# Performance work log

Measured on AMD Instinct MI355X. Metric: run time of the kernel, lower is better.

Reference implementation:

```python
import jax, jax.numpy as jnp
import numpy as np

EMBED_DIM = 1024
NUM_HEADS = 16
HEAD_DIM = EMBED_DIM // NUM_HEADS


def setup_inputs() -> dict:
    key = jax.random.key(0)
    ks = jax.random.split(key, 5)
    T, B, E = 2048, 2, EMBED_DIM
    s = 1.0 / np.sqrt(E)
    return {
        "x": jax.random.normal(ks[0], (T, B, E), jnp.float32),
        "wq": jax.random.normal(ks[1], (E, E), jnp.float32) * s,
        "bq": jnp.zeros((E,), jnp.float32),
        "wk": jax.random.normal(ks[2], (E, E), jnp.float32) * s,
        "bk": jnp.zeros((E,), jnp.float32),
        "wv": jax.random.normal(ks[3], (E, E), jnp.float32) * s,
        "bv": jnp.zeros((E,), jnp.float32),
        "wo": jax.random.normal(ks[4], (E, E), jnp.float32) * s,
        "bo": jnp.zeros((E,), jnp.float32),
    }


def reference(x, wq, bq, wk, bk, wv, bv, wo, bo):
    # x: [T, B, E] (Time x Batch x Channel), self-attention: query = key = value = x
    T, B, E = x.shape
    H, D = NUM_HEADS, HEAD_DIM
    scaling = D ** -0.5
    # Linear projections (torch Linear: y = x @ W.T + b)
    q = (jnp.einsum('tbe,fe->tbf', x, wq) + bq) * scaling
    k = jnp.einsum('tbe,fe->tbf', x, wk) + bk
    v = jnp.einsum('tbe,fe->tbf', x, wv) + bv
    # reshape to [B*H, T, D] equivalent -> use [B, H, T, D]
    q = q.reshape(T, B, H, D).transpose(1, 2, 0, 3)  # [B,H,T,D]
    k = k.reshape(T, B, H, D).transpose(1, 2, 0, 3)
    v = v.reshape(T, B, H, D).transpose(1, 2, 0, 3)
    # scores: [B,H,T,S], fp32 softmax
    scores = jnp.einsum('bhtd,bhsd->bhts', q, k)
    probs = jax.nn.softmax(scores.astype(jnp.float32), axis=-1).astype(x.dtype)
    attn = jnp.einsum('bhts,bhsd->bhtd', probs, v)  # [B,H,T,D]
    attn = attn.transpose(2, 0, 1, 3).reshape(T, B, E)
    out = jnp.einsum('tbe,fe->tbf', attn, wo) + bo
    return out
```

## Files before the change

### kernel.cpp

```cpp
#include <hip/hip_runtime.h>
#include <cstddef>
#include <cstdint>

#define T_DIM 2048
#define E_DIM 1024
#define M_DIM 4096

typedef __attribute__((ext_vector_type(8))) short short8;
typedef __attribute__((ext_vector_type(8))) _Float16 half8;
typedef __attribute__((ext_vector_type(4))) float f32x4;

__device__ __forceinline__ short f16_bits(float v) {
  return __builtin_bit_cast(short, (_Float16)v);
}
__device__ __forceinline__ unsigned int pk2(float a, float b) {
  return __builtin_bit_cast(unsigned int, __builtin_amdgcn_cvt_pkrtz(a, b));
}
__device__ __forceinline__ half8 h8(short8 s) { return __builtin_bit_cast(half8, s); }

__device__ __forceinline__ void gl_lds16(const short* g, const short* l) {
  __builtin_amdgcn_global_load_lds(
      (const __attribute__((address_space(1))) unsigned int*)g,
      (__attribute__((address_space(3))) unsigned int*)l, 16, 0, 0);
}

__global__ __launch_bounds__(256) void convert_all(
    const float* __restrict__ x, const float* __restrict__ wq,
    const float* __restrict__ wk, const float* __restrict__ wv,
    const float* __restrict__ wo,
    short* __restrict__ xh, short* __restrict__ wqh, short* __restrict__ wkh,
    short* __restrict__ wvh, short* __restrict__ woh)
{
  const int bid = blockIdx.x;
  const float* in; short* hi; int base;
  if (bid < 4096)      { in = x;  hi = xh;  base = 0;    }
  else if (bid < 5120) { in = wq; hi = wqh; base = 4096; }
  else if (bid < 6144) { in = wk; hi = wkh; base = 5120; }
  else if (bid < 7168) { in = wv; hi = wvh; base = 6144; }
  else                 { in = wo; hi = woh; base = 7168; }
  const int i = (bid - base) * 256 + threadIdx.x;
  float4 v = ((const float4*)in)[i];
  uint2 p;
  p.x = (unsigned short)f16_bits(v.x) | ((unsigned int)(unsigned short)f16_bits(v.y) << 16);
  p.y = (unsigned short)f16_bits(v.z) | ((unsigned int)(unsigned short)f16_bits(v.w) << 16);
  ((uint2*)hi)[i] = p;
}

__global__ __launch_bounds__(256) void gemm_qkv(
    const short* __restrict__ xh,
    const short* __restrict__ wqh, const short* __restrict__ wkh,
    const short* __restrict__ wvh,
    const float* __restrict__ bq, const float* __restrict__ bk,
    const float* __restrict__ bv,
    short* __restrict__ qo, short* __restrict__ ko, short* __restrict__ vto)
{
  __shared__ __align__(16) short smem[128 * 32 * 2];
  short* Ah = smem;
  short* Wh = smem + 128 * 32;
  const int tid = threadIdx.x;
  const int lane = tid & 63;
  const int w = tid >> 6;
  const int quad = lane >> 4;
  const int l15 = lane & 15;
  const int sel = blockIdx.x >> 3;
  const int n0 = (blockIdx.x & 7) * 128;
  const int m0 = blockIdx.y * 128;

  const short* wsel = sel == 0 ? wqh : sel == 1 ? wkh : wvh;
  const float* bias = sel == 0 ? bq : sel == 1 ? bk : bv;
  const float scale = sel == 0 ? 0.125f * 1.44269504088896f : 1.0f;

  const short* gsrc = (w < 2) ? xh : wsel;
  short* lbuf = (w < 2) ? Ah : Wh;
  const int rbase = (w < 2) ? m0 : n0;
  const int jb = (w & 1) * 4;
  const int lrow = lane >> 2;
  const int gphys = lane & 3;

  f32x4 zero = {0.f, 0.f, 0.f, 0.f};
  f32x4 acc[4][4];
#pragma unroll
  for (int i = 0; i < 4; ++i)
#pragma unroll
    for (int j = 0; j < 4; ++j) acc[i][j] = zero;

  const int wm = w & 1, wn = w >> 1;

  for (int k0 = 0; k0 < E_DIM; k0 += 32) {
    __syncthreads();
#pragma unroll
    for (int jj = 0; jj < 4; ++jj) {
      int j = jb + jj;
      int r = j * 16 + lrow;
      int gl = (gphys - (r >> 1)) & 3;
      gl_lds16(gsrc + (size_t)(rbase + r) * E_DIM + k0 + gl * 8, lbuf + j * 512);
    }
    __syncthreads();
    short8 ahf[4];
#pragma unroll
    for (int i = 0; i < 4; ++i) {
      int r = wm * 64 + i * 16 + l15;
      int idx = r * 32 + ((quad + (r >> 1)) & 3) * 8;
      ahf[i] = *(const short8*)&Ah[idx];
    }
#pragma unroll
    for (int j = 0; j < 4; ++j) {
      int r = wn * 64 + j * 16 + l15;
      int idx = r * 32 + ((quad + (r >> 1)) & 3) * 8;
      short8 bhf = *(const short8*)&Wh[idx];
#pragma unroll
      for (int i = 0; i < 4; ++i)
        acc[i][j] = __builtin_amdgcn_mfma_f32_16x16x32_f16(h8(ahf[i]), h8(bhf), acc[i][j], 0, 0, 0);
    }
  }

  if (sel < 2) {
#pragma unroll
    for (int j = 0; j < 4; ++j) {
      const int gc = n0 + wn * 64 + j * 16 + l15;
      const float bb = bias[gc];
      const int h = gc >> 6, d = gc & 63;
      short* dst = sel == 0 ? qo : ko;
#pragma unroll
      for (int i = 0; i < 4; ++i)
#pragma unroll
        for (int reg = 0; reg < 4; ++reg) {
          const int gm = m0 + wm * 64 + i * 16 + quad * 4 + reg;
          const float val = (acc[i][j][reg] + bb) * scale;
          const int t = gm >> 1, b = gm & 1;
          dst[((size_t)(b * 16 + h) * T_DIM + t) * 64 + d] = f16_bits(val);
        }
    }
  } else {
    short* Tb = smem;
    const int by = blockIdx.y;
#pragma unroll
    for (int R = 0; R < 2; ++R) {
      __syncthreads();
      if (wn == R) {
#pragma unroll
        for (int j = 0; j < 4; ++j) {
          const int nl = j * 16 + l15;
          const int gc = n0 + R * 64 + nl;
          const float bb = bias[gc];
#pragma unroll
          for (int i = 0; i < 4; ++i) {
            const int tp = wm * 32 + i * 8 + quad * 2;
            unsigned int lo = pk2(acc[i][j][0] + bb, acc[i][j][2] + bb);
            unsigned int hi = pk2(acc[i][j][1] + bb, acc[i][j][3] + bb);
            const int g0 = tp >> 3;
            const int sub = tp & 7;
            *(unsigned int*)&Tb[nl * 128 + ((g0 + nl) & 15) * 8 + sub] = lo;
            *(unsigned int*)&Tb[nl * 128 + ((g0 + 8 + nl) & 15) * 8 + sub] = hi;
          }
        }
      }
      __syncthreads();
#pragma unroll
      for (int ii = 0; ii < 4; ++ii) {
        const int n = w * 16 + ii * 4 + quad;
        const int g = (l15 - n) & 15;
        short8 vvec = *(const short8*)&Tb[n * 128 + l15 * 8];
        const int gc = n0 + R * 64 + n;
        const int h = gc >> 6, d = gc & 63;
        const int b = g >> 3;
        const int t = by * 64 + (g & 7) * 8;
        *(short8*)&vto[((size_t)(b * 16 + h) * 64 + d) * T_DIM + t] = vvec;
      }
    }
  }
}

__global__ __launch_bounds__(256) void gemm_out(
    const short* __restrict__ attn, const short* __restrict__ woh,
    const float* __restrict__ bo, float* __restrict__ out)
{
  __shared__ __align__(16) short Ah[128 * 32], Wh[128 * 32];
  const int tid = threadIdx.x;
  const int lane = tid & 63;
  const int w = tid >> 6;
  const int quad = lane >> 4;
  const int l15 = lane & 15;
  const int n0 = blockIdx.x * 128;
  const int m0 = blockIdx.y * 128;

  const short* gsrc = (w < 2) ? attn : woh;
  short* lbuf = (w < 2) ? Ah : Wh;
  const int rbase = (w < 2) ? m0 : n0;
  const int jb = (w & 1) * 4;
  const int lrow = lane >> 2;
  const int gphys = lane & 3;

  f32x4 zero = {0.f, 0.f, 0.f, 0.f};
  f32x4 acc[4][4];
#pragma unroll
  for (int i = 0; i < 4; ++i)
#pragma unroll
    for (int j = 0; j < 4; ++j) acc[i][j] = zero;

  const int wm = w & 1, wn = w >> 1;

  for (int k0 = 0; k0 < E_DIM; k0 += 32) {
    __syncthreads();
#pragma unroll
    for (int jj = 0; jj < 4; ++jj) {
      int j = jb + jj;
      int r = j * 16 + lrow;
      int gl = (gphys - (r >> 1)) & 3;
      gl_lds16(gsrc + (size_t)(rbase + r) * E_DIM + k0 + gl * 8, lbuf + j * 512);
    }
    __syncthreads();
    short8 ahf[4];
#pragma unroll
    for (int i = 0; i < 4; ++i) {
      int r = wm * 64 + i * 16 + l15;
      int idx = r * 32 + ((quad + (r >> 1)) & 3) * 8;
      ahf[i] = *(const short8*)&Ah[idx];
    }
#pragma unroll
    for (int j = 0; j < 4; ++j) {
      int r = wn * 64 + j * 16 + l15;
      int idx = r * 32 + ((quad + (r >> 1)) & 3) * 8;
      short8 bhf = *(const short8*)&Wh[idx];
#pragma unroll
      for (int i = 0; i < 4; ++i)
        acc[i][j] = __builtin_amdgcn_mfma_f32_16x16x32_f16(h8(ahf[i]), h8(bhf), acc[i][j], 0, 0, 0);
    }
  }

#pragma unroll
  for (int j = 0; j < 4; ++j) {
    const int gc = n0 + wn * 64 + j * 16 + l15;
    const float bb = bo[gc];
#pragma unroll
    for (int i = 0; i < 4; ++i)
#pragma unroll
      for (int reg = 0; reg < 4; ++reg) {
        const int gm = m0 + wm * 64 + i * 16 + quad * 4 + reg;
        out[(size_t)gm * E_DIM + gc] = acc[i][j][reg] + bb;
      }
  }
}

__global__ __launch_bounds__(256, 3) void attn_mfma(
    const short* __restrict__ q, const short* __restrict__ k,
    const short* __restrict__ vt, short* __restrict__ attn)
{
  __shared__ __align__(16) short QP[128 * 64];
  __shared__ __align__(16) short Ks[2][64 * 64], Vs[2][64 * 64];
  __shared__ float l_lds[4][128];

  const int tid = threadIdx.x;
  const int lane = tid & 63;
  const int w = tid >> 6;
  const int quad = lane >> 4;
  const int l15 = lane & 15;
  const int bhid = blockIdx.y;
  const int b = bhid >> 4, h = bhid & 15;
  const int t0 = blockIdx.x * 128;

  const short* qb = q + (size_t)bhid * T_DIM * 64;
  const short* kb = k + (size_t)bhid * T_DIM * 64;
  const short* vb = vt + (size_t)bhid * 64 * T_DIM;

  const int lrow8 = lane >> 3;
  const int gph8 = lane & 7;

#pragma unroll
  for (int jj = 0; jj < 4; ++jj) {
    int j = w * 4 + jj;
    int r = j * 8 + lrow8;
    int gl = (gph8 - (r >> 1)) & 7;
    gl_lds16(qb + (size_t)(t0 + r) * 64 + gl * 8, QP + j * 512);
  }
#pragma unroll
  for (int jj = 0; jj < 2; ++jj) {
    int j = w * 2 + jj;
    int r = j * 8 + lrow8;
    int gl = (gph8 - (r >> 1)) & 7;
    gl_lds16(kb + (size_t)r * 64 + gl * 8, Ks[0] + j * 512);
    gl_lds16(vb + (size_t)r * T_DIM + 0 + gl * 8, Vs[0] + j * 512);
  }
  __syncthreads();

  short8 qa[8][2];
#pragma unroll
  for (int qbk = 0; qbk < 8; ++qbk)
#pragma unroll
    for (int st = 0; st < 2; ++st) {
      int r = qbk * 16 + l15;
      int idx = r * 64 + (((st * 4 + quad) + (r >> 1)) & 7) * 8;
      qa[qbk][st] = *(const short8*)&QP[idx];
    }
  __syncthreads();

  f32x4 zero = {0.f, 0.f, 0.f, 0.f};
  f32x4 acc[4][2];
  float l_part[8];
#pragma unroll
  for (int d = 0; d < 4; ++d) { acc[d][0] = zero; acc[d][1] = zero; }
#pragma unroll
  for (int i = 0; i < 8; ++i) l_part[i] = 0.f;

  for (int c = 0; c < 32; ++c) {
    const int cur = c & 1;
    if (c < 31) {
      const int s0n = (c + 1) * 64;
#pragma unroll
      for (int jj = 0; jj < 2; ++jj) {
        int j = w * 2 + jj;
        int r = j * 8 + lrow8;
        int gl = (gph8 - (r >> 1)) & 7;
        gl_lds16(kb + (size_t)(s0n + r) * 64 + gl * 8, Ks[cur ^ 1] + j * 512);
        gl_lds16(vb + (size_t)r * T_DIM + s0n + gl * 8, Vs[cur ^ 1] + j * 512);
      }
    }

    short8 kf[2];
#pragma unroll
    for (int st = 0; st < 2; ++st) {
      int r = w * 16 + l15;
      int idx = r * 64 + (((st * 4 + quad) + (r >> 1)) & 7) * 8;
      kf[st] = *(const short8*)&Ks[cur][idx];
    }
#pragma unroll
    for (int qbk = 0; qbk < 8; ++qbk) {
      f32x4 s = zero;
      s = __builtin_amdgcn_mfma_f32_16x16x32_f16(h8(kf[0]), h8(qa[qbk][0]), s, 0, 0, 0);
      s = __builtin_amdgcn_mfma_f32_16x16x32_f16(h8(kf[1]), h8(qa[qbk][1]), s, 0, 0, 0);
      float p0 = __builtin_amdgcn_exp2f(s[0]);
      float p1 = __builtin_amdgcn_exp2f(s[1]);
      float p2 = __builtin_amdgcn_exp2f(s[2]);
      float p3 = __builtin_amdgcn_exp2f(s[3]);
      l_part[qbk] += (p0 + p1) + (p2 + p3);
      const int qq = qbk * 16 + l15;
      const int g = w * 2 + (quad >> 1);
      const int gp = (g + (qq >> 1)) & 7;
      uint2 pw; pw.x = pk2(p0, p1); pw.y = pk2(p2, p3);
      *(uint2*)&QP[qq * 64 + gp * 8 + (quad & 1) * 4] = pw;
    }
    __syncthreads();

    short8 pb[2][2];
#pragma unroll
    for (int qb2 = 0; qb2 < 2; ++qb2)
#pragma unroll
      for (int st = 0; st < 2; ++st) {
        int qq = w * 32 + qb2 * 16 + l15;
        int idx = qq * 64 + (((st * 4 + quad) + (qq >> 1)) & 7) * 8;
        pb[qb2][st] = *(const short8*)&QP[idx];
      }
#pragma unroll
    for (int dblk = 0; dblk < 4; ++dblk) {
      short8 vf[2];
#pragma unroll
      for (int st = 0; st < 2; ++st) {
        int r = dblk * 16 + l15;
        int idx = r * 64 + (((st * 4 + quad) + (r >> 1)) & 7) * 8;
        vf[st] = *(const short8*)&Vs[cur][idx];
      }
#pragma unroll
      for (int qb2 = 0; qb2 < 2; ++qb2) {
        acc[dblk][qb2] = __builtin_amdgcn_mfma_f32_16x16x32_f16(h8(vf[0]), h8(pb[qb2][0]), acc[dblk][qb2], 0, 0, 0);
        acc[dblk][qb2] = __builtin_amdgcn_mfma_f32_16x16x32_f16(h8(vf[1]), h8(pb[qb2][1]), acc[dblk][qb2], 0, 0, 0);
      }
    }
    __syncthreads();
  }

#pragma unroll
  for (int qbk = 0; qbk < 8; ++qbk) {
    float l = l_part[qbk];
    l += __shfl_xor(l, 16);
    l += __shfl_xor(l, 32);
    if (quad == 0) l_lds[w][qbk * 16 + l15] = l;
  }
  __syncthreads();

#pragma unroll
  for (int qb2 = 0; qb2 < 2; ++qb2) {
    const int qq = w * 32 + qb2 * 16 + l15;
    const float lsum = l_lds[0][qq] + l_lds[1][qq] + l_lds[2][qq] + l_lds[3][qq];
    const float inv = 1.f / lsum;
    const int t = t0 + qq;
    const size_t mrow = (size_t)(t * 2 + b) * E_DIM;
#pragma unroll
    for (int dblk = 0; dblk < 4; ++dblk) {
      uint2 ov;
      ov.x = pk2(acc[dblk][qb2][0] * inv, acc[dblk][qb2][1] * inv);
      ov.y = pk2(acc[dblk][qb2][2] * inv, acc[dblk][qb2][3] * inv);
      *(uint2*)&attn[mrow + h * 64 + dblk * 16 + quad * 4] = ov;
    }
  }
}

extern "C" void kernel_launch(void* const* d_in, const int* in_sizes, int n_in,
                              void* d_out, int out_size, void* d_ws, size_t ws_size,
                              hipStream_t stream)
{
  const float* x  = (const float*)d_in[0];
  const float* wq = (const float*)d_in[1];
  const float* bq = (const float*)d_in[2];
  const float* wk = (const float*)d_in[3];
  const float* bk = (const float*)d_in[4];
  const float* wv = (const float*)d_in[5];
  const float* bv = (const float*)d_in[6];
  const float* wo = (const float*)d_in[7];
  const float* bo = (const float*)d_in[8];
  float* out = (float*)d_out;

  short* ws = (short*)d_ws;
  const size_t M4 = (size_t)M_DIM * E_DIM;
  const size_t M1 = (size_t)E_DIM * E_DIM;
  short* xh   = ws;
  short* wqh  = xh + M4;
  short* wkh  = wqh + M1;
  short* wvh  = wkh + M1;
  short* woh  = wvh + M1;
  short* qws  = woh + M1;
  short* kws  = qws + M4;
  short* vtws = kws + M4;
  short* aws  = vtws + M4;

  convert_all<<<8192, 256, 0, stream>>>(x, wq, wk, wv, wo, xh, wqh, wkh, wvh, woh);
  gemm_qkv<<<dim3(24, 32), 256, 0, stream>>>(xh, wqh, wkh, wvh, bq, bk, bv,
                                             qws, kws, vtws);
  attn_mfma<<<dim3(16, 32), 256, 0, stream>>>(qws, kws, vtws, aws);
  gemm_out<<<dim3(8, 32), 256, 0, stream>>>(aws, woh, bo, out);
}
```

Baseline: 206.0 us.

## Keep P in registers, split keys per wave, triple-buffer KV with waitcnt

```diff
diff --git a/kernel.cpp b/kernel.cpp
--- a/kernel.cpp
+++ b/kernel.cpp
@@ -8,6 +8,7 @@
 
 typedef __attribute__((ext_vector_type(8))) short short8;
 typedef __attribute__((ext_vector_type(8))) _Float16 half8;
+typedef __attribute__((ext_vector_type(4))) _Float16 half4;
 typedef __attribute__((ext_vector_type(4))) float f32x4;
 
 __device__ __forceinline__ short f16_bits(float v) {
@@ -242,13 +243,14 @@
   }
 }
 
-__global__ __launch_bounds__(256, 3) void attn_mfma(
+__global__ __launch_bounds__(256, 2) void attn_mfma(
     const short* __restrict__ q, const short* __restrict__ k,
     const short* __restrict__ vt, short* __restrict__ attn)
 {
-  __shared__ __align__(16) short QP[128 * 64];
-  __shared__ __align__(16) short Ks[2][64 * 64], Vs[2][64 * 64];
-  __shared__ float l_lds[4][128];
+  __shared__ __align__(16) short SMEM[32768];
+  __shared__ float l_red[4][128];
+  short* Qs = SMEM;
+  short* KV = SMEM + 8192;
 
   const int tid = threadIdx.x;
   const int lane = tid & 63;
@@ -271,15 +273,19 @@
     int j = w * 4 + jj;
     int r = j * 8 + lrow8;
     int gl = (gph8 - (r >> 1)) & 7;
-    gl_lds16(qb + (size_t)(t0 + r) * 64 + gl * 8, QP + j * 512);
-  }
-#pragma unroll
-  for (int jj = 0; jj < 2; ++jj) {
-    int j = w * 2 + jj;
-    int r = j * 8 + lrow8;
-    int gl = (gph8 - (r >> 1)) & 7;
-    gl_lds16(kb + (size_t)r * 64 + gl * 8, Ks[0] + j * 512);
-    gl_lds16(vb + (size_t)r * T_DIM + 0 + gl * 8, Vs[0] + j * 512);
+    gl_lds16(qb + (size_t)(t0 + r) * 64 + gl * 8, Qs + j * 512);
+  }
+
+  const int kg = (gph8 - lrow8) & 7;
+  const int vd = lane >> 1, vh = lane & 1;
+#pragma unroll
+  for (int c0 = 0; c0 < 2; ++c0) {
+    short* slot = KV + c0 * 8192 + w * 2048;
+    const int sg = c0 * 64 + w * 16;
+    gl_lds16(kb + (size_t)(sg + lrow8) * 64 + kg * 8, slot);
+    gl_lds16(kb + (size_t)(sg + lrow8 + 8) * 64 + kg * 8, slot + 512);
+    gl_lds16(vb + (size_t)vd * T_DIM + sg + vh * 8, slot + 1024);
+    gl_lds16(vb + (size_t)(vd + 32) * T_DIM + sg + vh * 8, slot + 1536);
   }
   __syncthreads();
 
@@ -290,39 +296,45 @@
     for (int st = 0; st < 2; ++st) {
       int r = qbk * 16 + l15;
       int idx = r * 64 + (((st * 4 + quad) + (r >> 1)) & 7) * 8;
-      qa[qbk][st] = *(const short8*)&QP[idx];
-    }
-  __syncthreads();
+      qa[qbk][st] = *(const short8*)&Qs[idx];
+    }
 
   f32x4 zero = {0.f, 0.f, 0.f, 0.f};
-  f32x4 acc[4][2];
+  f32x4 acc[4][8];
   float l_part[8];
 #pragma unroll
-  for (int d = 0; d < 4; ++d) { acc[d][0] = zero; acc[d][1] = zero; }
+  for (int d = 0; d < 4; ++d)
+#pragma unroll
+    for (int qb2 = 0; qb2 < 8; ++qb2) acc[d][qb2] = zero;
 #pragma unroll
   for (int i = 0; i < 8; ++i) l_part[i] = 0.f;
 
   for (int c = 0; c < 32; ++c) {
-    const int cur = c & 1;
-    if (c < 31) {
-      const int s0n = (c + 1) * 64;
-#pragma unroll
-      for (int jj = 0; jj < 2; ++jj) {
-        int j = w * 2 + jj;
-        int r = j * 8 + lrow8;
-        int gl = (gph8 - (r >> 1)) & 7;
-        gl_lds16(kb + (size_t)(s0n + r) * 64 + gl * 8, Ks[cur ^ 1] + j * 512);
-        gl_lds16(vb + (size_t)r * T_DIM + s0n + gl * 8, Vs[cur ^ 1] + j * 512);
-      }
-    }
+    if (c >= 2) {
+      if (c == 31) __builtin_amdgcn_s_waitcnt(0x0F70);
+      else         __builtin_amdgcn_s_waitcnt(0x0F74);
+    }
+    const short* slot = KV + (c % 3) * 8192 + w * 2048;
 
     short8 kf[2];
 #pragma unroll
-    for (int st = 0; st < 2; ++st) {
-      int r = w * 16 + l15;
-      int idx = r * 64 + (((st * 4 + quad) + (r >> 1)) & 7) * 8;
-      kf[st] = *(const short8*)&Ks[cur][idx];
-    }
+    for (int st = 0; st < 2; ++st)
+      kf[st] = *(const short8*)&slot[l15 * 64 + (((st * 4 + quad) + l15) & 7) * 8];
+    uint2 vfu[4];
+#pragma unroll
+    for (int dblk = 0; dblk < 4; ++dblk)
+      vfu[dblk] = *(const uint2*)&slot[1024 + (dblk * 16 + l15) * 16 + quad * 4];
+
+    if (c < 30) {
+      short* nslot = KV + ((c + 2) % 3) * 8192 + w * 2048;
+      const int sg = (c + 2) * 64 + w * 16;
+      gl_lds16(kb + (size_t)(sg + lrow8) * 64 + kg * 8, nslot);
+      gl_lds16(kb + (size_t)(sg + lrow8 + 8) * 64 + kg * 8, nslot + 512);
+      gl_lds16(vb + (size_t)vd * T_DIM + sg + vh * 8, nslot + 1024);
+      gl_lds16(vb + (size_t)(vd + 32) * T_DIM + sg + vh * 8, nslot + 1536);
+    }
+
+    uint2 pb[8];
 #pragma unroll
     for (int qbk = 0; qbk < 8; ++qbk) {
       f32x4 s = zero;
@@ -333,39 +345,18 @@
       float p2 = __builtin_amdgcn_exp2f(s[2]);
       float p3 = __builtin_amdgcn_exp2f(s[3]);
       l_part[qbk] += (p0 + p1) + (p2 + p3);
-      const int qq = qbk * 16 + l15;
-      const int g = w * 2 + (quad >> 1);
-      const int gp = (g + (qq >> 1)) & 7;
-      uint2 pw; pw.x = pk2(p0, p1); pw.y = pk2(p2, p3);
-      *(uint2*)&QP[qq * 64 + gp * 8 + (quad & 1) * 4] = pw;
-    }
-    __syncthreads();
-
-    short8 pb[2][2];
-#pragma unroll
-    for (int qb2 = 0; qb2 < 2; ++qb2)
-#pragma unroll
-      for (int st = 0; st < 2; ++st) {
-        int qq = w * 32 + qb2 * 16 + l15;
-        int idx = qq * 64 + (((st * 4 + quad) + (qq >> 1)) & 7) * 8;
-        pb[qb2][st] = *(const short8*)&QP[idx];
-      }
+      pb[qbk].x = pk2(p0, p1);
+      pb[qbk].y = pk2(p2, p3);
+    }
+
 #pragma unroll
     for (int dblk = 0; dblk < 4; ++dblk) {
-      short8 vf[2];
-#pragma unroll
-      for (int st = 0; st < 2; ++st) {
-        int r = dblk * 16 + l15;
-        int idx = r * 64 + (((st * 4 + quad) + (r >> 1)) & 7) * 8;
-        vf[st] = *(const short8*)&Vs[cur][idx];
-      }
-#pragma unroll
-      for (int qb2 = 0; qb2 < 2; ++qb2) {
-        acc[dblk][qb2] = __builtin_amdgcn_mfma_f32_16x16x32_f16(h8(vf[0]), h8(pb[qb2][0]), acc[dblk][qb2], 0, 0, 0);
-        acc[dblk][qb2] = __builtin_amdgcn_mfma_f32_16x16x32_f16(h8(vf[1]), h8(pb[qb2][1]), acc[dblk][qb2], 0, 0, 0);
-      }
-    }
-    __syncthreads();
+      half4 va = __builtin_bit_cast(half4, vfu[dblk]);
+#pragma unroll
+      for (int qbk = 0; qbk < 8; ++qbk)
+        acc[dblk][qbk] = __builtin_amdgcn_mfma_f32_16x16x16f16(
+            va, __builtin_bit_cast(half4, pb[qbk]), acc[dblk][qbk], 0, 0, 0);
+    }
   }
 
 #pragma unroll
@@ -373,23 +364,60 @@
     float l = l_part[qbk];
     l += __shfl_xor(l, 16);
     l += __shfl_xor(l, 32);
-    if (quad == 0) l_lds[w][qbk * 16 + l15] = l;
-  }
+    if (quad == 0) l_red[w][qbk * 16 + l15] = l;
+  }
+
+  f32x4* Osc = (f32x4*)SMEM;
   __syncthreads();
-
-#pragma unroll
-  for (int qb2 = 0; qb2 < 2; ++qb2) {
-    const int qq = w * 32 + qb2 * 16 + l15;
-    const float lsum = l_lds[0][qq] + l_lds[1][qq] + l_lds[2][qq] + l_lds[3][qq];
-    const float inv = 1.f / lsum;
-    const int t = t0 + qq;
-    const size_t mrow = (size_t)(t * 2 + b) * E_DIM;
-#pragma unroll
-    for (int dblk = 0; dblk < 4; ++dblk) {
-      uint2 ov;
-      ov.x = pk2(acc[dblk][qb2][0] * inv, acc[dblk][qb2][1] * inv);
-      ov.y = pk2(acc[dblk][qb2][2] * inv, acc[dblk][qb2][3] * inv);
-      *(uint2*)&attn[mrow + h * 64 + dblk * 16 + quad * 4] = ov;
+  if (w & 1) {
+    f32x4* dst = Osc + (w >> 1) * 2048;
+#pragma unroll
+    for (int dblk = 0; dblk < 4; ++dblk)
+#pragma unroll
+      for (int qbk = 0; qbk < 8; ++qbk)
+        dst[(dblk * 8 + qbk) * 64 + lane] = acc[dblk][qbk];
+  }
+  __syncthreads();
+  if (!(w & 1)) {
+    f32x4* src = Osc + (w >> 1) * 2048;
+#pragma unroll
+    for (int dblk = 0; dblk < 4; ++dblk)
+#pragma unroll
+      for (int qbk = 0; qbk < 8; ++qbk) {
+        f32x4 t = src[(dblk * 8 + qbk) * 64 + lane];
+        acc[dblk][qbk][0] += t[0]; acc[dblk][qbk][1] += t[1];
+        acc[dblk][qbk][2] += t[2]; acc[dblk][qbk][3] += t[3];
+      }
+  }
+  __syncthreads();
+  if (w == 2) {
+#pragma unroll
+    for (int dblk = 0; dblk < 4; ++dblk)
+#pragma unroll
+      for (int qbk = 0; qbk < 8; ++qbk)
+        Osc[(dblk * 8 + qbk) * 64 + lane] = acc[dblk][qbk];
+  }
+  __syncthreads();
+  if (w == 0) {
+#pragma unroll
+    for (int qbk = 0; qbk < 8; ++qbk) {
+      const int qq = qbk * 16 + l15;
+      const float lsum = l_red[0][qq] + l_red[1][qq] + l_red[2][qq] + l_red[3][qq];
+      const float inv = 1.f / lsum;
+      const int t = t0 + qq;
+      const size_t mrow = (size_t)(t * 2 + b) * E_DIM;
+#pragma unroll
+      for (int dblk = 0; dblk < 4; ++dblk) {
+        f32x4 t4 = Osc[(dblk * 8 + qbk) * 64 + lane];
+        float a0 = acc[dblk][qbk][0] + t4[0];
+        float a1 = acc[dblk][qbk][1] + t4[1];
+        float a2 = acc[dblk][qbk][2] + t4[2];
+        float a3 = acc[dblk][qbk][3] + t4[3];
+        uint2 ov;
+        ov.x = pk2(a0 * inv, a1 * inv);
+        ov.y = pk2(a2 * inv, a3 * inv);
+        *(uint2*)&attn[mrow + h * 64 + dblk * 16 + quad * 4] = ov;
+      }
     }
   }
 }
```

New measurement: 202.8 us. No clear change (-1.5%).
